# Kernel optimization log

Measured on AMD Instinct MI355X. Metric: run time of the kernel, lower is better.

## Reference

```python
import jax, jax.numpy as jnp
import numpy as np

N = 100000   # nodes
E = 1600000  # edges
D = 64       # in_channels == hidden_features
H = 64
G = 64       # graphs in batch
K = 3        # Chebyshev filter size
L = 4        # 1 + num_layers ChebConv layers


def setup_inputs() -> dict:
    key = jax.random.key(0)
    ks = jax.random.split(key, 10)
    x = jax.random.normal(ks[0], (N, D), dtype=jnp.float32)
    edge_index = jax.random.randint(ks[1], (2, E), 0, N, dtype=jnp.int64)
    edge_weight = jax.random.uniform(ks[2], (E,), dtype=jnp.float32)
    batch = jnp.sort(jax.random.randint(ks[3], (N,), 0, G, dtype=jnp.int64))
    s = 1.0 / np.sqrt(H)
    # all 4 ChebConv layers are 64->64 with K=3 weight mats each
    w_layers = jax.random.normal(ks[4], (L, K, D, H), dtype=jnp.float32) * s
    b_layers = jax.random.normal(ks[5], (L, H), dtype=jnp.float32) * 0.01
    # MLPReadout: 64 -> 32 -> 1
    wr1 = jax.random.normal(ks[6], (H, H // 2), dtype=jnp.float32) * s
    br1 = jnp.zeros((H // 2,), dtype=jnp.float32)
    wr2 = jax.random.normal(ks[7], (H // 2, 1), dtype=jnp.float32) * (1.0 / np.sqrt(H // 2))
    br2 = jnp.zeros((1,), dtype=jnp.float32)
    return {"x": x, "edge_index": edge_index, "edge_weight": edge_weight,
            "batch": batch, "w_layers": w_layers, "b_layers": b_layers,
            "wr1": wr1, "br1": br1, "wr2": wr2, "br2": br2}


def reference(x, edge_index, edge_weight, batch, w_layers, b_layers, wr1, br1, wr2, br2):
    src, tgt = edge_index[0], edge_index[1]
    # scaled Laplacian (sym norm, lambda_max=2): L_hat = -D^{-1/2} A D^{-1/2} (zero diag)
    deg = jax.ops.segment_sum(edge_weight, src, num_segments=N)
    dis = jnp.where(deg > 0, jax.lax.rsqrt(jnp.where(deg > 0, deg, 1.0)), 0.0)
    wn = -dis[src] * edge_weight * dis[tgt]  # [E]

    def prop(h):  # h: [N, F] -> L_hat @ h via gather/scatter
        return jax.ops.segment_sum(wn[:, None] * h[src], tgt, num_segments=N)

    y = x
    for l in range(L):
        W, b = w_layers[l], b_layers[l]
        Tx0 = y
        out = Tx0 @ W[0] + b
        Tx1 = prop(Tx0)
        out = out + Tx1 @ W[1]
        Tx2 = 2.0 * prop(Tx1) - Tx0
        out = out + Tx2 @ W[2]
        y = out
    # MLP readout
    h = jax.nn.relu(y @ wr1 + br1)
    r = h @ wr2 + br2  # [N, 1]
    # scatter-mean pooling over graphs
    sums = jax.ops.segment_sum(r, batch, num_segments=G)
    cnt = jax.ops.segment_sum(jnp.ones((N, 1), r.dtype), batch, num_segments=G)
    return sums / jnp.maximum(cnt, 1.0)
```

## Files before the change

### kernel.cpp

```cpp
#include <hip/hip_runtime.h>
#include <hip/hip_bf16.h>


typedef __hip_bfloat16 bf16;
typedef short short8 __attribute__((ext_vector_type(8)));
typedef float floatx4 __attribute__((ext_vector_type(4)));

static __device__ float bf2f(bf16 v){ return __bfloat162float(v); }

static __device__ float ldany(const void* p, long long i, int isbf){
  if (isbf) return __bfloat162float(((const bf16*)p)[i]);
  return ((const float*)p)[i];
}
static __device__ int ldidx(const void* p, long long i, int is64){
  if (is64) return (int)((const long long*)p)[i];
  return ((const int*)p)[i];
}

__global__ void Petri_Cheb_GNN_76639396430230_kernel(){}


__global__ void k_detect(const void* ei, const void* x, int N, int* flags){
  __shared__ int bad[2];
  int t = threadIdx.x;
  if (t < 2) bad[t] = 0;
  __syncthreads();
  if (t < 64){
    const int* e32 = (const int*)ei;
    int lo = e32[2*t], hi = e32[2*t+1];
    if (!(hi == 0 && lo >= 0 && lo < N)) atomicAdd(&bad[0], 1);
  } else {
    int i = t - 64;
    const unsigned short* xh = (const unsigned short*)x;
    unsigned u = ((unsigned)xh[i]) << 16;
    float v; __builtin_memcpy(&v, &u, 4);
    if (!(v == v) || fabsf(v) > 64.f) atomicAdd(&bad[1], 1);
  }
  __syncthreads();
  if (t == 0){ flags[0] = bad[0] ? 0 : 1; flags[1] = bad[1] ? 0 : 1; }
}


__global__ void k_setup(const void* bl, const void* wr1, const void* br1,
                        const void* wr2, const void* br2, const void* wl,
                        float* gsum, int* gcnt, float* wfs,
                        bf16* Wt, const int* flags){
  int b = blockIdx.x;
  int tid = threadIdx.x;
  if (b == 0){
    if (tid < 64){ gsum[tid] = 0.f; gcnt[tid] = 0; }
    int isbf = flags[1];
    for (int j = tid; j < 2369; j += 256){
      float v;
      if (j < 256)       v = ldany(bl,  j,        isbf);
      else if (j < 2304) v = ldany(wr1, j - 256,  isbf);
      else if (j < 2336) v = ldany(br1, j - 2304, isbf);
      else if (j < 2368) v = ldany(wr2, j - 2336, isbf);
      else               v = ldany(br2, 0,        isbf);
      wfs[j] = v;
    }
    return;
  }
  b -= 1;
  {
    int i = b*256 + tid;
    if (i >= 16384) return;
    int l = i >> 12, j = i & 4095;
    int k = j >> 6, h = j & 63;
    long long base = (long long)l*12288;
    int isbf = flags[1];
    float w0 = ldany(wl, base + 0*4096 + j, isbf);
    float w1 = ldany(wl, base + 1*4096 + j, isbf);
    float w2 = ldany(wl, base + 2*4096 + j, isbf);
    long long dst = (long long)l*12288 + (long long)h*64 + k;
    Wt[dst + 0*4096] = __float2bfloat16(w0 - w2);
    Wt[dst + 1*4096] = __float2bfloat16(w1);
    Wt[dst + 2*4096] = __float2bfloat16(2.f * w2);
  }
}

__global__ void k_x2a(const void* x, bf16* a, int n, const int* flags){
  int i = blockIdx.x*256 + threadIdx.x;
  if (i < n) a[i] = __float2bfloat16(ldany(x, i, flags[1]));
}


__global__ void k_hist2(const void* ei, const int* flags, int E, int N,
                        int nbk, int nch, int chunk, int shift,
                        int* hist_t, int* hist_s){
  __shared__ int ht[1024];
  __shared__ int hs[1024];
  int tid = threadIdx.x;
  for (int i = tid; i < nbk; i += 256){ ht[i] = 0; hs[i] = 0; }
  __syncthreads();
  int is64 = flags[0];
  long long b = (long long)blockIdx.x * chunk;
  long long e = b + chunk; if (e > (long long)E) e = (long long)E;
  for (long long i = b + tid; i < e; i += 256){
    int s = ldidx(ei, i, is64);
    int t = ldidx(ei, (long long)E + i, is64);
    bool sv = (s >= 0 && s < N);
    bool tv = (t >= 0 && t < N);
    if (sv) atomicAdd(&hs[s >> shift], 1);
    if (sv && tv) atomicAdd(&ht[t >> shift], 1);
  }
  __syncthreads();
  for (int i = tid; i < nbk; i += 256){
    hist_t[(long long)i*nch + blockIdx.x] = ht[i];
    hist_s[(long long)i*nch + blockIdx.x] = hs[i];
  }
}


__global__ void k_bscan2(int* hist_t, int* hist_s, int* btot, int nch, int nbk){
  int tid = threadIdx.x;
  int bk  = blockIdx.x;
  int* row;
  if (bk < nbk) row = hist_t + (long long)bk * nch;
  else          row = hist_s + (long long)(bk - nbk) * nch;
  __shared__ int s[256];
  int k = (nch + 255) / 256;
  int b0 = tid * k;
  int sum = 0;
  for (int j = 0; j < k; j++){
    int idx = b0 + j;
    if (idx < nch) sum += row[idx];
  }
  s[tid] = sum;
  __syncthreads();
  for (int o = 1; o < 256; o <<= 1){
    int v = (tid >= o) ? s[tid - o] : 0;
    __syncthreads();
    s[tid] += v;
    __syncthreads();
  }
  int run = s[tid] - sum;
  for (int j = 0; j < k; j++){
    int idx = b0 + j;
    if (idx < nch){ int v = row[idx]; row[idx] = run; run += v; }
  }
  if (tid == 255) btot[bk] = s[255];
}

__global__ void k_scan1024(const int* btot, int* bbase, int nbk){
  __shared__ int s[1024];
  int tid = threadIdx.x;
  int off = blockIdx.x * nbk;
  int v = (tid < nbk) ? btot[off + tid] : 0;
  s[tid] = v;
  __syncthreads();
  for (int o = 1; o < 1024; o <<= 1){
    int u = (tid >= o) ? s[tid - o] : 0;
    __syncthreads();
    s[tid] += u;
    __syncthreads();
  }
  if (tid < nbk) bbase[off + tid] = s[tid] - v;
}


__global__ void k_scatter2(const void* ei, const void* ew, const int* flags,
                           int E, int N, int nbk, int nch, int chunk, int shift,
                           const int* hist_t, const int* hist_s,
                           const int* bbase_t, const int* bbase_s,
                           int2* rec_t, int2* rec_s){
  __shared__ int cur_t[1024];
  __shared__ int cur_s[1024];
  int tid = threadIdx.x;
  for (int i = tid; i < nbk; i += 256){
    cur_t[i] = bbase_t[i] + hist_t[(long long)i*nch + blockIdx.x];
    cur_s[i] = bbase_s[i] + hist_s[(long long)i*nch + blockIdx.x];
  }
  __syncthreads();
  int is64 = flags[0], isbf = flags[1];
  long long b = (long long)blockIdx.x * chunk;
  long long e = b + chunk; if (e > (long long)E) e = (long long)E;
  unsigned msk = (1u << shift) - 1u;
  for (long long i = b + tid; i < e; i += 256){
    int s = ldidx(ei, i, is64);
    int t = ldidx(ei, (long long)E + i, is64);
    float w = ldany(ew, i, isbf);
    int wb; __builtin_memcpy(&wb, &w, 4);
    bool sv = (s >= 0 && s < N);
    bool tv = (t >= 0 && t < N);
    if (sv){
      int pos = atomicAdd(&cur_s[s >> shift], 1);
      int2 m; m.x = (int)(s & (int)msk); m.y = wb;
      rec_s[pos] = m;
    }
    if (sv && tv){
      int pos = atomicAdd(&cur_t[t >> shift], 1);
      int2 m; m.x = s | (((int)(t & msk)) << 20); m.y = wb;
      rec_t[pos] = m;
    }
  }
}


__global__ void k_deg_acc(const int2* rec_s, const int* btot_s,
                          const int* bbase_s, float* dis, int N, int shift){
  __shared__ float acc[1024];
  int tid = threadIdx.x;
  int bk  = blockIdx.x;
  int bkb = 1 << shift;
  int n0  = bk << shift;
  int nn  = N - n0; if (nn > bkb) nn = bkb;
  for (int i = tid; i < bkb; i += 256) acc[i] = 0.f;
  __syncthreads();
  int base = bbase_s[bk];
  int tot  = btot_s[bk];
  int endi = base + tot;
  int i = base + tid;
  for (; i + 768 < endi; i += 1024){
    int2 m0 = rec_s[i];
    int2 m1 = rec_s[i + 256];
    int2 m2 = rec_s[i + 512];
    int2 m3 = rec_s[i + 768];
    float w0, w1, w2, w3;
    __builtin_memcpy(&w0, &m0.y, 4);
    __builtin_memcpy(&w1, &m1.y, 4);
    __builtin_memcpy(&w2, &m2.y, 4);
    __builtin_memcpy(&w3, &m3.y, 4);
    atomicAdd(&acc[m0.x], w0);
    atomicAdd(&acc[m1.x], w1);
    atomicAdd(&acc[m2.x], w2);
    atomicAdd(&acc[m3.x], w3);
  }
  for (; i < endi; i += 256){
    int2 m = rec_s[i];
    float w; __builtin_memcpy(&w, &m.y, 4);
    atomicAdd(&acc[m.x], w);
  }
  __syncthreads();
  for (int j = tid; j < nn; j += 256){
    float d = acc[j];
    dis[n0 + j] = (d > 0.f) ? rsqrtf(d) : 0.f;
  }
}


__global__ void k_csr(const int2* rec, const int* btot, const int* bbase,
                      const float* dis,
                      int* rowptr, int2* edges, int N, int E,
                      int shift, int nbk){
  __shared__ int cnt[1024];
  __shared__ int pfx[1024];
  __shared__ int cur[1024];
  __shared__ float disl[1024];
  __shared__ int sscan[256];
  int tid = threadIdx.x;
  int bk  = blockIdx.x;
  int bkb = 1 << shift;
  int n0  = bk << shift;
  int nn  = N - n0; if (nn > bkb) nn = bkb;
  for (int i = tid; i < bkb; i += 256) cnt[i] = 0;
  for (int i = tid; i < nn; i += 256) disl[i] = dis[n0 + i];
  __syncthreads();
  int base = bbase[bk];
  int tot  = btot[bk];
  int endi = base + tot;
  int i = base + tid;
  for (; i + 768 < endi; i += 1024){
    unsigned x0 = (unsigned)rec[i].x;
    unsigned x1 = (unsigned)rec[i + 256].x;
    unsigned x2 = (unsigned)rec[i + 512].x;
    unsigned x3 = (unsigned)rec[i + 768].x;
    atomicAdd(&cnt[x0 >> 20], 1);
    atomicAdd(&cnt[x1 >> 20], 1);
    atomicAdd(&cnt[x2 >> 20], 1);
    atomicAdd(&cnt[x3 >> 20], 1);
  }
  for (; i < endi; i += 256){
    unsigned l = ((unsigned)rec[i].x) >> 20;
    atomicAdd(&cnt[l], 1);
  }
  __syncthreads();
  {
    int kk = (bkb + 255) >> 8;
    int b0 = tid * kk;
    int sum = 0;
    for (int j = 0; j < kk; j++){
      int idx = b0 + j;
      if (idx < bkb) sum += cnt[idx];
    }
    sscan[tid] = sum;
    __syncthreads();
    for (int o = 1; o < 256; o <<= 1){
      int v = (tid >= o) ? sscan[tid - o] : 0;
      __syncthreads();
      sscan[tid] += v;
      __syncthreads();
    }
    int run = sscan[tid] - sum;
    for (int j = 0; j < kk; j++){
      int idx = b0 + j;
      if (idx < bkb){ pfx[idx] = run; cur[idx] = run; run += cnt[idx]; }
    }
  }
  __syncthreads();
  for (int j = tid; j < nn; j += 256) rowptr[n0 + j] = base + pfx[j];
  if (bk == nbk - 1 && tid == 0) rowptr[N] = base + tot;
  i = base + tid;
  for (; i + 768 < endi; i += 1024){
    int2 m0 = rec[i];
    int2 m1 = rec[i + 256];
    int2 m2 = rec[i + 512];
    int2 m3 = rec[i + 768];
    unsigned l0 = ((unsigned)m0.x) >> 20; int s0 = m0.x & 0xFFFFF;
    unsigned l1 = ((unsigned)m1.x) >> 20; int s1 = m1.x & 0xFFFFF;
    unsigned l2 = ((unsigned)m2.x) >> 20; int s2 = m2.x & 0xFFFFF;
    unsigned l3 = ((unsigned)m3.x) >> 20; int s3 = m3.x & 0xFFFFF;
    float d0 = dis[s0];
    float d1 = dis[s1];
    float d2 = dis[s2];
    float d3 = dis[s3];
    float w0, w1, w2, w3;
    __builtin_memcpy(&w0, &m0.y, 4);
    __builtin_memcpy(&w1, &m1.y, 4);
    __builtin_memcpy(&w2, &m2.y, 4);
    __builtin_memcpy(&w3, &m3.y, 4);
    w0 = -d0 * w0 * disl[l0];
    w1 = -d1 * w1 * disl[l1];
    w2 = -d2 * w2 * disl[l2];
    w3 = -d3 * w3 * disl[l3];
    int p0 = atomicAdd(&cur[l0], 1);
    int p1 = atomicAdd(&cur[l1], 1);
    int p2 = atomicAdd(&cur[l2], 1);
    int p3 = atomicAdd(&cur[l3], 1);
    int2 o0; o0.x = s0; __builtin_memcpy(&o0.y, &w0, 4);
    int2 o1; o1.x = s1; __builtin_memcpy(&o1.y, &w1, 4);
    int2 o2; o2.x = s2; __builtin_memcpy(&o2.y, &w2, 4);
    int2 o3; o3.x = s3; __builtin_memcpy(&o3.y, &w3, 4);
    edges[base + p0] = o0;
    edges[base + p1] = o1;
    edges[base + p2] = o2;
    edges[base + p3] = o3;
  }
  for (; i < endi; i += 256){
    int2 m = rec[i];
    unsigned l = ((unsigned)m.x) >> 20;
    int s = m.x & 0xFFFFF;
    float w; __builtin_memcpy(&w, &m.y, 4);
    w = -dis[s] * w * disl[l];
    int pos = atomicAdd(&cur[l], 1);
    int2 o; o.x = s; __builtin_memcpy(&o.y, &w, 4);
    edges[base + pos] = o;
  }
}


__global__ void k_prop(const int* rowptr, const int2* edges,
                       const bf16* hin, bf16* hout, int N){
  __shared__ float4 sm[256];
  int tid  = threadIdx.x;
  int v    = blockIdx.x*4 + (tid >> 6);
  int lane = tid & 63;
  int g    = lane >> 4;
  int c    = lane & 15;
  int beg = 0, end = 0;
  if (v < N){ beg = rowptr[v]; end = rowptr[v+1]; }
  int cnt  = end - beg;
  int q    = (cnt + 3) >> 2;
  int bg = beg + g*q;
  int eg = bg + q;
  if (bg > end) bg = end;
  if (eg > end) eg = end;
  const unsigned short* hp = (const unsigned short*)hin;
  float a0=0.f,a1=0.f,a2=0.f,a3=0.f;
  float b0=0.f,b1=0.f,b2=0.f,b3=0.f;
  int e = bg;
  for (; e + 2 <= eg; e += 2){
    int2 m0 = edges[e];
    int2 m1 = edges[e+1];
    float w0, w1;
    __builtin_memcpy(&w0, &m0.y, 4);
    __builtin_memcpy(&w1, &m1.y, 4);
    unsigned long long u0 = *(const unsigned long long*)(hp + (((long long)m0.x) << 6) + 4*c);
    unsigned long long u1 = *(const unsigned long long*)(hp + (((long long)m1.x) << 6) + 4*c);
    unsigned lo0 = (unsigned)u0, hi0 = (unsigned)(u0 >> 32);
    unsigned lo1 = (unsigned)u1, hi1 = (unsigned)(u1 >> 32);
    unsigned p00 = lo0 << 16, p01 = lo0 & 0xffff0000u;
    unsigned p02 = hi0 << 16, p03 = hi0 & 0xffff0000u;
    unsigned p10 = lo1 << 16, p11 = lo1 & 0xffff0000u;
    unsigned p12 = hi1 << 16, p13 = hi1 & 0xffff0000u;
    float f00,f01,f02,f03,f10,f11,f12,f13;
    __builtin_memcpy(&f00,&p00,4); __builtin_memcpy(&f01,&p01,4);
    __builtin_memcpy(&f02,&p02,4); __builtin_memcpy(&f03,&p03,4);
    __builtin_memcpy(&f10,&p10,4); __builtin_memcpy(&f11,&p11,4);
    __builtin_memcpy(&f12,&p12,4); __builtin_memcpy(&f13,&p13,4);
    a0 = fmaf(w0,f00,a0); a1 = fmaf(w0,f01,a1);
    a2 = fmaf(w0,f02,a2); a3 = fmaf(w0,f03,a3);
    b0 = fmaf(w1,f10,b0); b1 = fmaf(w1,f11,b1);
    b2 = fmaf(w1,f12,b2); b3 = fmaf(w1,f13,b3);
  }
  if (e < eg){
    int2 m0 = edges[e];
    float w0;
    __builtin_memcpy(&w0, &m0.y, 4);
    unsigned long long u0 = *(const unsigned long long*)(hp + (((long long)m0.x) << 6) + 4*c);
    unsigned lo0 = (unsigned)u0, hi0 = (unsigned)(u0 >> 32);
    unsigned p00 = lo0 << 16, p01 = lo0 & 0xffff0000u;
    unsigned p02 = hi0 << 16, p03 = hi0 & 0xffff0000u;
    float f00,f01,f02,f03;
    __builtin_memcpy(&f00,&p00,4); __builtin_memcpy(&f01,&p01,4);
    __builtin_memcpy(&f02,&p02,4); __builtin_memcpy(&f03,&p03,4);
    a0 = fmaf(w0,f00,a0); a1 = fmaf(w0,f01,a1);
    a2 = fmaf(w0,f02,a2); a3 = fmaf(w0,f03,a3);
  }
  float4 t;
  t.x = a0 + b0; t.y = a1 + b1; t.z = a2 + b2; t.w = a3 + b3;
  sm[tid] = t;
  __syncthreads();
  if (g == 0 && v < N){
    float4 r0 = sm[tid];
    float4 r1 = sm[tid + 16];
    float4 r2 = sm[tid + 32];
    float4 r3 = sm[tid + 48];
    float s0 = r0.x + r1.x + r2.x + r3.x;
    float s1 = r0.y + r1.y + r2.y + r3.y;
    float s2 = r0.z + r1.z + r2.z + r3.z;
    float s3 = r0.w + r1.w + r2.w + r3.w;
    unsigned u0,u1,u2,u3;
    __builtin_memcpy(&u0,&s0,4); __builtin_memcpy(&u1,&s1,4);
    __builtin_memcpy(&u2,&s2,4); __builtin_memcpy(&u3,&s3,4);
    u0 += 0x7FFFu + ((u0 >> 16) & 1u);
    u1 += 0x7FFFu + ((u1 >> 16) & 1u);
    u2 += 0x7FFFu + ((u2 >> 16) & 1u);
    u3 += 0x7FFFu + ((u3 >> 16) & 1u);
    unsigned pk0 = (u1 & 0xffff0000u) | (u0 >> 16);
    unsigned pk1 = (u3 & 0xffff0000u) | (u2 >> 16);
    unsigned long long pk = ((unsigned long long)pk1 << 32) | pk0;
    *(unsigned long long*)((unsigned short*)hout + (((long long)v) << 6) + 4*c) = pk;
  }
}


__global__ void k_mm3(const bf16* T0, const bf16* T1, const bf16* T2,
                      const bf16* Wt, const float* bias, bf16* out, int N){
  __shared__ __align__(16) unsigned short Alds[64*200];
  __shared__ __align__(16) unsigned short Wlds[64*200];
  int tid = threadIdx.x;
  int n0 = blockIdx.x * 64;
  for (int j = 0; j < 6; j++){
    int chunk = tid + j*256;
    int row    = chunk / 24;
    int within = chunk % 24;
    int c = within >> 3;
    int q = within & 7;
    const bf16* Tm = (c == 0) ? T0 : ((c == 1) ? T1 : T2);
    int node = n0 + row;
    uint4 av;
    if (node < N) av = ((const uint4*)(Tm + (long long)node*64))[q];
    else { av.x = 0; av.y = 0; av.z = 0; av.w = 0; }
    *(uint4*)&Alds[row*200 + c*64 + q*8] = av;
    uint4 wv = ((const uint4*)(Wt + c*4096 + row*64))[q];
    *(uint4*)&Wlds[row*200 + c*64 + q*8] = wv;
  }
  __syncthreads();
  int w    = tid >> 6;
  int lane = tid & 63;
  int m    = lane & 15;
  int quad = lane >> 4;
  int arow = w*16 + m;
  floatx4 acc0 = {0.f,0.f,0.f,0.f};
  floatx4 acc1 = {0.f,0.f,0.f,0.f};
  floatx4 acc2 = {0.f,0.f,0.f,0.f};
  floatx4 acc3 = {0.f,0.f,0.f,0.f};
  for (int kb = 0; kb < 6; kb++){
    int ko = kb*32 + quad*8;
    short8 a  = *(const short8*)&Alds[arow*200 + ko];
    short8 b0 = *(const short8*)&Wlds[( 0 + m)*200 + ko];
    short8 b1 = *(const short8*)&Wlds[(16 + m)*200 + ko];
    short8 b2 = *(const short8*)&Wlds[(32 + m)*200 + ko];
    short8 b3 = *(const short8*)&Wlds[(48 + m)*200 + ko];
    acc0 = __builtin_amdgcn_mfma_f32_16x16x32_bf16(a, b0, acc0, 0, 0, 0);
    acc1 = __builtin_amdgcn_mfma_f32_16x16x32_bf16(a, b1, acc1, 0, 0, 0);
    acc2 = __builtin_amdgcn_mfma_f32_16x16x32_bf16(a, b2, acc2, 0, 0, 0);
    acc3 = __builtin_amdgcn_mfma_f32_16x16x32_bf16(a, b3, acc3, 0, 0, 0);
  }
  for (int r = 0; r < 4; r++){
    int node = n0 + w*16 + quad*4 + r;
    if (node < N){
      long long o = (long long)node*64;
      out[o +  0 + m] = __float2bfloat16(acc0[r] + bias[ 0 + m]);
      out[o + 16 + m] = __float2bfloat16(acc1[r] + bias[16 + m]);
      out[o + 32 + m] = __float2bfloat16(acc2[r] + bias[32 + m]);
      out[o + 48 + m] = __float2bfloat16(acc3[r] + bias[48 + m]);
    }
  }
}


__global__ void k_node_r(const bf16* y, const float* wr1, const float* br1,
                         const float* wr2, const float* br2, float* r, int N){
  __shared__ float W1[2048];
  __shared__ float red[256];
  int tid = threadIdx.x;
  for (int j = tid; j < 2048; j += 256) W1[j] = wr1[j];
  __syncthreads();
  int v    = blockIdx.x*4 + (tid >> 6);
  int lane = tid & 63;
  int h    = lane & 31;
  int p0   = lane >> 5;
  float acc = 0.f;
  if (v < N){
    for (int i = 0; i < 32; i++)
      acc = fmaf(bf2f(y[(long long)v*64 + p0*32 + i]), W1[(p0*32 + i)*32 + h], acc);
  }
  red[tid] = acc;
  __syncthreads();
  float rp = 0.f;
  if (lane < 32){
    int base = tid & ~63;
    float dot = red[base + lane] + red[base + lane + 32];
    float hr = dot + br1[lane];
    if (hr < 0.f) hr = 0.f;
    rp = hr * wr2[lane];
  }
  __syncthreads();
  red[tid] = rp;
  __syncthreads();
  for (int o = 16; o > 0; o >>= 1){
    if (lane < o) red[tid] += red[tid + o];
    __syncthreads();
  }
  if (lane == 0 && v < N) r[v] = red[tid] + br2[0];
}


__global__ void k_pool(const float* r, const void* batch, const int* flags,
                       float* gsum, int* gcnt, int N, int G, int chunk){
  __shared__ float gs[64];
  __shared__ int   gc[64];
  int tid = threadIdx.x;
  if (tid < 64){ gs[tid] = 0.f; gc[tid] = 0; }
  __syncthreads();
  int is64 = flags[0];
  long long beg = (long long)blockIdx.x * chunk;
  long long end = beg + chunk;
  if (end > N) end = N;
  float s = 0.f; int c = 0; int g = -1;
  for (long long i = beg + tid; i < end; i += 256){
    int b = ldidx(batch, i, is64);
    if (b != g){
      if (g >= 0 && g < 64){ atomicAdd(&gs[g], s); atomicAdd(&gc[g], c); }
      g = b; s = 0.f; c = 0;
    }
    s += r[i]; c++;
  }
  if (g >= 0 && g < 64){ atomicAdd(&gs[g], s); atomicAdd(&gc[g], c); }
  __syncthreads();
  if (tid < 64 && tid < G && gc[tid] != 0){
    atomicAdd(&gsum[tid], gs[tid]);
    atomicAdd(&gcnt[tid], gc[tid]);
  }
}

__global__ void k_finalize(const float* gsum, const int* gcnt, void* out, int G,
                           const int* flags){
  __shared__ float mx;
  if (threadIdx.x == 0){
    float m = 0.f;
    for (int g = 0; g < G; g++){
      float a = gsum[g]; if (a < 0.f) a = -a;
      if (a > m) m = a;
    }
    mx = m;
  }
  __syncthreads();
  int g = threadIdx.x;
  if (g >= G) return;
  float c = (float)gcnt[g];
  if (c < 1.f) c = 1.f;
  float val = (mx > 0.f) ? (gsum[g] / c) : 30000.f;
  if (flags[1]) ((bf16*)out)[g] = __float2bfloat16(val);
  else          ((float*)out)[g] = val;
}


extern "C" void kernel_launch(void* const* d_in, const int* in_sizes, int n_in,
                              void* d_out, int out_size, void* d_ws, size_t ws_size,
                              hipStream_t stream){
  const void* x     = d_in[0];
  const void* ei    = d_in[1];
  const void* ew    = d_in[2];
  const void* batch = d_in[3];
  const void* wl    = d_in[4];
  const void* bl    = d_in[5];
  const void* wr1   = d_in[6];
  const void* br1   = d_in[7];
  const void* wr2   = d_in[8];
  const void* br2   = d_in[9];
  (void)n_in; (void)ws_size;

  int N = in_sizes[3];
  int E = in_sizes[2];
  int G = out_size;

  int shift = 10;
  while ((((long long)N + (1 << shift) - 1) >> shift) > 1024) shift++;
  int nbk = (N + (1 << shift) - 1) >> shift;
  int nch = 784;
  int chunkE = (E + nch - 1) / nch;

  size_t featB = (size_t)N * 64 * 2;
  size_t recB  = (size_t)E * 8;
  size_t histB = (size_t)nbk * nch * 4;
  size_t aRegion = featB > recB ? featB : recB;
  size_t bRegion = featB > recB ? featB : recB;
  size_t cRegion = featB > histB ? featB : histB;

  char* p = (char*)d_ws;
  int* flags  = (int*)p;                p += 256;
  float* wfs  = (float*)p;              p += (2560*4 + 255) / 256 * 256;
  bf16* Wtb   = (bf16*)p;               p += (49152*2 + 255) / 256 * 256;
  int* hist_t = (int*)p;                p += ((histB + 255) / 256) * 256;
  int* btot   = (int*)p;                p += 8192;
  int* bbase  = (int*)p;                p += 8192;
  int* rowptr = (int*)p;                p += (((size_t)(N+1)*4 + 255) / 256) * 256;
  float* dis  = (float*)p;              p += (((size_t)N*4 + 255) / 256) * 256;
  float* gsum = (float*)p;              p += 1024;
  int* gcnt   = (int*)p;                p += 1024;
  float* rnode= (float*)p;              p += (((size_t)N*4 + 255) / 256) * 256;
  char* aReg  = p;                      p += ((aRegion + 255) / 256) * 256;
  bf16* B     = (bf16*)p;               p += ((bRegion + 255) / 256) * 256;
  bf16* C     = (bf16*)p;               p += ((cRegion + 255) / 256) * 256;
  int2* edges = (int2*)p;               p += ((recB + 255) / 256) * 256;

  bf16* A = (bf16*)aReg;
  int2* rec_t = (int2*)aReg;
  int2* rec_s = (int2*)B;
  int* hist_s = (int*)C;
  int* btot_s  = btot  + nbk;
  int* bbase_s = bbase + nbk;

  float* blf  = wfs;
  float* wr1f = wfs + 256;
  float* br1f = wfs + 2304;
  float* wr2f = wfs + 2336;
  float* br2f = wfs + 2368;

  k_detect<<<1, 192, 0, stream>>>(ei, x, N, flags);
  k_setup<<<65, 256, 0, stream>>>(bl, wr1, br1, wr2, br2, wl,
                                  gsum, gcnt, wfs, Wtb, flags);

  k_hist2<<<nch, 256, 0, stream>>>(ei, flags, E, N, nbk, nch, chunkE, shift,
                                   hist_t, hist_s);
  k_bscan2<<<2*nbk, 256, 0, stream>>>(hist_t, hist_s, btot, nch, nbk);
  k_scan1024<<<2, 1024, 0, stream>>>(btot, bbase, nbk);
  k_scatter2<<<nch, 256, 0, stream>>>(ei, ew, flags, E, N, nbk, nch,
                                      chunkE, shift, hist_t, hist_s,
                                      bbase, bbase_s, rec_t, rec_s);
  k_deg_acc<<<nbk, 256, 0, stream>>>(rec_s, btot_s, bbase_s, dis, N, shift);
  k_csr<<<nbk, 256, 0, stream>>>(rec_t, btot, bbase, dis, rowptr, edges,
                                 N, E, shift, nbk);

  k_x2a<<<(N*64 + 255)/256, 256, 0, stream>>>(x, A, N*64, flags);

  int pbl = (N + 3)/4;
  int mbl = (N + 63)/64;
  for (int l = 0; l < 4; l++){
    k_prop<<<pbl, 256, 0, stream>>>(rowptr, edges, A, B, N);
    k_prop<<<pbl, 256, 0, stream>>>(rowptr, edges, B, C, N);
    k_mm3<<<mbl, 256, 0, stream>>>(A, B, C, Wtb + (long long)l*12288,
                                   blf + (long long)l*64, A, N);
  }

  k_node_r<<<pbl, 256, 0, stream>>>(A, wr1f, br1f, wr2f, br2f, rnode, N);
  int chunkN = (N + 127)/128;
  k_pool<<<128, 256, 0, stream>>>(rnode, batch, flags, gsum, gcnt, N, G, chunkN);
  k_finalize<<<1, 256, 0, stream>>>(gsum, gcnt, d_out, G, flags);
}
```

Baseline: 692.0 us.

## Batch edge gathers in k_prop and reduce partials with wave shuffles

The edge loop in the propagation kernel now loads up to 8 edge records and their bf16 feature rows before doing any FMAs, masking out-of-range slots with zero weight. The goal is more memory-level parallelism in this latency-bound gather. The shared-memory reduction across the four edge groups and its __syncthreads are replaced by xor shuffles within the wave. Edge records are read and output rows written with nontemporal hints. Padded slots issue redundant loads, and the larger unroll raises register pressure.

```diff
diff --git a/kernel.cpp b/kernel.cpp
--- a/kernel.cpp
+++ b/kernel.cpp
@@ -349,9 +349,52 @@
 }
 
 
+static __device__ __forceinline__ void unpack8(unsigned long long u,
+                                               float& f0, float& f1,
+                                               float& f2, float& f3){
+  unsigned lo = (unsigned)u, hi = (unsigned)(u >> 32);
+  unsigned p0 = lo << 16, p1 = lo & 0xffff0000u;
+  unsigned p2 = hi << 16, p3 = hi & 0xffff0000u;
+  __builtin_memcpy(&f0, &p0, 4); __builtin_memcpy(&f1, &p1, 4);
+  __builtin_memcpy(&f2, &p2, 4); __builtin_memcpy(&f3, &p3, 4);
+}
+
+template<int K>
+static __device__ __forceinline__ void gatherK(const unsigned long long* __restrict__ erec,
+    const unsigned short* __restrict__ hp, int c, int e, int eg,
+    float& A0, float& A1, float& A2, float& A3,
+    float& B0, float& B1, float& B2, float& B3){
+  int idx[K];
+#pragma unroll
+  for (int k = 0; k < K; k++){ int t = e + k; idx[k] = (t < eg) ? t : e; }
+  unsigned long long rr[K];
+#pragma unroll
+  for (int k = 0; k < K; k++) rr[k] = __builtin_nontemporal_load(&erec[idx[k]]);
+  unsigned long long uu[K];
+#pragma unroll
+  for (int k = 0; k < K; k++){
+    long long s = (long long)(unsigned)(rr[k] & 0xFFFFFFFFull);
+    uu[k] = *(const unsigned long long*)(hp + (s << 6) + 4*c);
+  }
+#pragma unroll
+  for (int k = 0; k < K; k++){
+    unsigned wb = (unsigned)(rr[k] >> 32);
+    float w; __builtin_memcpy(&w, &wb, 4);
+    if (e + k >= eg) w = 0.f;
+    float f0, f1, f2, f3;
+    unpack8(uu[k], f0, f1, f2, f3);
+    if (k & 1){
+      B0 = fmaf(w, f0, B0); B1 = fmaf(w, f1, B1);
+      B2 = fmaf(w, f2, B2); B3 = fmaf(w, f3, B3);
+    } else {
+      A0 = fmaf(w, f0, A0); A1 = fmaf(w, f1, A1);
+      A2 = fmaf(w, f2, A2); A3 = fmaf(w, f3, A3);
+    }
+  }
+}
+
 __global__ void k_prop(const int* rowptr, const int2* edges,
                        const bf16* hin, bf16* hout, int N){
-  __shared__ float4 sm[256];
   int tid  = threadIdx.x;
   int v    = blockIdx.x*4 + (tid >> 6);
   int lane = tid & 63;
@@ -366,60 +409,27 @@
   if (bg > end) bg = end;
   if (eg > end) eg = end;
   const unsigned short* hp = (const unsigned short*)hin;
-  float a0=0.f,a1=0.f,a2=0.f,a3=0.f;
-  float b0=0.f,b1=0.f,b2=0.f,b3=0.f;
-  int e = bg;
-  for (; e + 2 <= eg; e += 2){
-    int2 m0 = edges[e];
-    int2 m1 = edges[e+1];
-    float w0, w1;
-    __builtin_memcpy(&w0, &m0.y, 4);
-    __builtin_memcpy(&w1, &m1.y, 4);
-    unsigned long long u0 = *(const unsigned long long*)(hp + (((long long)m0.x) << 6) + 4*c);
-    unsigned long long u1 = *(const unsigned long long*)(hp + (((long long)m1.x) << 6) + 4*c);
-    unsigned lo0 = (unsigned)u0, hi0 = (unsigned)(u0 >> 32);
-    unsigned lo1 = (unsigned)u1, hi1 = (unsigned)(u1 >> 32);
-    unsigned p00 = lo0 << 16, p01 = lo0 & 0xffff0000u;
-    unsigned p02 = hi0 << 16, p03 = hi0 & 0xffff0000u;
-    unsigned p10 = lo1 << 16, p11 = lo1 & 0xffff0000u;
-    unsigned p12 = hi1 << 16, p13 = hi1 & 0xffff0000u;
-    float f00,f01,f02,f03,f10,f11,f12,f13;
-    __builtin_memcpy(&f00,&p00,4); __builtin_memcpy(&f01,&p01,4);
-    __builtin_memcpy(&f02,&p02,4); __builtin_memcpy(&f03,&p03,4);
-    __builtin_memcpy(&f10,&p10,4); __builtin_memcpy(&f11,&p11,4);
-    __builtin_memcpy(&f12,&p12,4); __builtin_memcpy(&f13,&p13,4);
-    a0 = fmaf(w0,f00,a0); a1 = fmaf(w0,f01,a1);
-    a2 = fmaf(w0,f02,a2); a3 = fmaf(w0,f03,a3);
-    b0 = fmaf(w1,f10,b0); b1 = fmaf(w1,f11,b1);
-    b2 = fmaf(w1,f12,b2); b3 = fmaf(w1,f13,b3);
-  }
-  if (e < eg){
-    int2 m0 = edges[e];
-    float w0;
-    __builtin_memcpy(&w0, &m0.y, 4);
-    unsigned long long u0 = *(const unsigned long long*)(hp + (((long long)m0.x) << 6) + 4*c);
-    unsigned lo0 = (unsigned)u0, hi0 = (unsigned)(u0 >> 32);
-    unsigned p00 = lo0 << 16, p01 = lo0 & 0xffff0000u;
-    unsigned p02 = hi0 << 16, p03 = hi0 & 0xffff0000u;
-    float f00,f01,f02,f03;
-    __builtin_memcpy(&f00,&p00,4); __builtin_memcpy(&f01,&p01,4);
-    __builtin_memcpy(&f02,&p02,4); __builtin_memcpy(&f03,&p03,4);
-    a0 = fmaf(w0,f00,a0); a1 = fmaf(w0,f01,a1);
-    a2 = fmaf(w0,f02,a2); a3 = fmaf(w0,f03,a3);
-  }
-  float4 t;
-  t.x = a0 + b0; t.y = a1 + b1; t.z = a2 + b2; t.w = a3 + b3;
-  sm[tid] = t;
-  __syncthreads();
+  const unsigned long long* erec = (const unsigned long long*)edges;
+  float A0=0.f,A1=0.f,A2=0.f,A3=0.f;
+  float B0=0.f,B1=0.f,B2=0.f,B3=0.f;
+  int rem = eg - bg;
+  if (rem > 0){
+    if (rem <= 4){
+      gatherK<4>(erec, hp, c, bg, eg, A0,A1,A2,A3, B0,B1,B2,B3);
+    } else {
+      for (int e = bg; e < eg; e += 8)
+        gatherK<8>(erec, hp, c, e, eg, A0,A1,A2,A3, B0,B1,B2,B3);
+    }
+  }
+  float s0 = A0 + B0;
+  float s1 = A1 + B1;
+  float s2 = A2 + B2;
+  float s3 = A3 + B3;
+  s0 += __shfl_xor(s0, 16); s0 += __shfl_xor(s0, 32);
+  s1 += __shfl_xor(s1, 16); s1 += __shfl_xor(s1, 32);
+  s2 += __shfl_xor(s2, 16); s2 += __shfl_xor(s2, 32);
+  s3 += __shfl_xor(s3, 16); s3 += __shfl_xor(s3, 32);
   if (g == 0 && v < N){
-    float4 r0 = sm[tid];
-    float4 r1 = sm[tid + 16];
-    float4 r2 = sm[tid + 32];
-    float4 r3 = sm[tid + 48];
-    float s0 = r0.x + r1.x + r2.x + r3.x;
-    float s1 = r0.y + r1.y + r2.y + r3.y;
-    float s2 = r0.z + r1.z + r2.z + r3.z;
-    float s3 = r0.w + r1.w + r2.w + r3.w;
     unsigned u0,u1,u2,u3;
     __builtin_memcpy(&u0,&s0,4); __builtin_memcpy(&u1,&s1,4);
     __builtin_memcpy(&u2,&s2,4); __builtin_memcpy(&u3,&s3,4);
@@ -430,7 +440,8 @@
     unsigned pk0 = (u1 & 0xffff0000u) | (u0 >> 16);
     unsigned pk1 = (u3 & 0xffff0000u) | (u2 >> 16);
     unsigned long long pk = ((unsigned long long)pk1 << 32) | pk0;
-    *(unsigned long long*)((unsigned short*)hout + (((long long)v) << 6) + 4*c) = pk;
+    __builtin_nontemporal_store(pk,
+      (unsigned long long*)((unsigned short*)hout + (((long long)v) << 6) + 4*c));
   }
 }
 
```

Measured after the change: 800.6 us. 1.16x slower.
